# Performance work log

Hardware: AMD Instinct MI355X
Metric: run time of the kernel (lower is better)

Reference implementation:

```python
import jax, jax.numpy as jnp
import numpy as np

G = 8  # order of C8 rotation group

def expand_circulant(w):
    # w: [out_fields, in_fields, G] free params of a C8 regular->regular 1x1 conv.
    # Full weight: W[of*G+go, if*G+gi] = w[of, if, (go-gi) mod G]
    g = jnp.arange(G)
    idx = (g[:, None] - g[None, :]) % G            # [go, gi]
    Wf = w[:, :, idx]                              # [of, if, go, gi]
    Wf = jnp.transpose(Wf, (0, 2, 1, 3))           # [of, go, if, gi]
    return Wf.reshape(w.shape[0] * G, w.shape[1] * G)

def eq_proj(x2, w, b):
    # x2: [B, in_fields*G]; equivariant 1x1 conv = GEMM with circulant-expanded weight
    Wf = expand_circulant(w)                       # [out_fields*G, in_fields*G]
    bf = jnp.repeat(b, G)                          # per-field bias, shared across group dim
    return x2 @ Wf.T + bf

def setup_inputs() -> dict:
    key = jax.random.key(0)
    ks = jax.random.split(key, 12)
    B, d_model, n_head, d_k, d_v = 8192, 128, 8, 64, 64
    C = d_model * G                                # 1024
    s_in = 0.02
    inp = {
        'q': jax.random.normal(ks[0], (B, C, 1, 1), jnp.float32),
        'k': jax.random.normal(ks[1], (B, C, 1, 1), jnp.float32),
        'v': jax.random.normal(ks[2], (B, C, 1, 1), jnp.float32),
        'w_q': jax.random.normal(ks[3], (n_head * d_k, d_model, G), jnp.float32) * s_in,
        'b_q': jnp.zeros((n_head * d_k,), jnp.float32),
        'w_k': jax.random.normal(ks[4], (n_head * d_k, d_model, G), jnp.float32) * s_in,
        'b_k': jnp.zeros((n_head * d_k,), jnp.float32),
        'w_v': jax.random.normal(ks[5], (n_head * d_v, d_model, G), jnp.float32) * s_in,
        'b_v': jnp.zeros((n_head * d_v,), jnp.float32),
        'w_fc': jax.random.normal(ks[6], (d_model, n_head * d_v, G), jnp.float32) * s_in,
        'b_fc': jnp.zeros((d_model,), jnp.float32),
    }
    return inp

def reference(q, k, v, w_q, b_q, w_k, b_k, w_v, b_v, w_fc, b_fc):
    B, C = q.shape[0], q.shape[1]
    n_head, d_k = 8, 64
    d_v = 64
    temp = jnp.asarray(d_k ** 0.5, q.dtype)
    residual = q                                   # [B, C, 1, 1]
    q2 = q.reshape(B, C)
    k2 = k.reshape(B, C)
    v2 = v.reshape(B, C)
    # equivariant 1x1 conv projections -> [B, n_head*d_k*G]
    qp = eq_proj(q2, w_q, b_q).reshape(B, G, n_head, d_k).transpose(0, 2, 1, 3)  # [B,H,G,dk]
    kp = eq_proj(k2, w_k, b_k).reshape(B, G, n_head, d_k).transpose(0, 2, 1, 3)
    vp = eq_proj(v2, w_v, b_v).reshape(B, G, n_head, d_v).transpose(0, 2, 1, 3)
    # scaled dot-product attention over the G=8 group/orientation positions
    attn = jax.nn.softmax(jnp.einsum('bhqd,bhkd->bhqk', qp / temp, kp), axis=-1)  # [B,H,G,G]
    out = jnp.einsum('bhqk,bhkd->bhqd', attn, vp)  # [B,H,G,dv]
    # transpose(1,2) then flatten, exactly as torch .view(sz_b, -1, 1, 1)
    out = out.transpose(0, 2, 1, 3).reshape(B, G * n_head * d_v)
    out = eq_proj(out, w_fc, b_fc)                 # [B, d_model*G]
    out = out.reshape(B, C, 1, 1) + residual
    return out, attn
```

## Files before the change

### kernel.cpp

```cpp
#include <hip/hip_runtime.h>
#include <hip/hip_bf16.h>

typedef unsigned short u16;
typedef unsigned int u32;
typedef __bf16 bf16x8_t __attribute__((ext_vector_type(8)));
typedef float f32x4_t __attribute__((ext_vector_type(4)));

#define BK 64

__device__ __forceinline__ float b2f(u16 v) {
  return __uint_as_float(((u32)v) << 16);
}
__device__ __forceinline__ u16 f2b(float f) {
  __hip_bfloat16 h = __float2bfloat16(f);
  return *reinterpret_cast<u16*>(&h);
}
__device__ __forceinline__ float blo(u32 u) { return __uint_as_float(u << 16); }
__device__ __forceinline__ float bhi(u32 u) { return __uint_as_float(u & 0xffff0000u); }

__device__ __forceinline__ void async_lds16(const u16* g, u16* l) {
  __builtin_amdgcn_global_load_lds(
      (__attribute__((address_space(1))) void*)g,
      (__attribute__((address_space(3))) void*)l, 16, 0, 0);
}

__device__ __forceinline__ void expand8(const float* __restrict__ w,
                                        u16* __restrict__ dst, int I,
                                        int kshift, int gid) {
  const int n = gid >> kshift;
  const int kc = (gid & ((1 << kshift) - 1)) * 8;
  const int K = 8 << kshift;
  const float* wp = w + (size_t)((n >> 3) * I + (kc >> 3)) * 8;
  float4 w0 = *(const float4*)wp;
  float4 w1 = *(const float4*)(wp + 4);
  float w8[8] = {w0.x, w0.y, w0.z, w0.w, w1.x, w1.y, w1.z, w1.w};
  u16 t[8];
  const int r = (n - kc) & 7;
#pragma unroll
  for (int j = 0; j < 8; ++j) t[j] = f2b(w8[(r - j) & 7]);
  *(uint4*)(dst + (size_t)n * K + kc) = *(const uint4*)t;
}

__device__ __forceinline__ void cvt8(const float* __restrict__ src,
                                     u16* __restrict__ dst, int gid) {
  const float* p = src + (size_t)gid * 8;
  float4 a = *(const float4*)p;
  float4 b = *(const float4*)(p + 4);
  u16 t[8] = {f2b(a.x), f2b(a.y), f2b(a.z), f2b(a.w),
              f2b(b.x), f2b(b.y), f2b(b.z), f2b(b.w)};
  *(uint4*)(dst + (size_t)gid * 8) = *(const uint4*)t;
}

__global__ __launch_bounds__(256) void expand_all(
    const float* __restrict__ w_q, const float* __restrict__ w_k,
    const float* __restrict__ w_v, const float* __restrict__ w_fc,
    const float* __restrict__ q, const float* __restrict__ k,
    const float* __restrict__ v, u16* __restrict__ Wq, u16* __restrict__ Wk,
    u16* __restrict__ Wv, u16* __restrict__ Wfc, u16* __restrict__ qb,
    u16* __restrict__ kb, u16* __restrict__ vb, int cblocks) {
  const int e = blockIdx.x;
  if (e < 8192) {
    const int plane = e >> 11;
    const int gid = (e & 2047) * 256 + threadIdx.x;
    if (plane == 0) expand8(w_q, Wq, 128, 7, gid);
    else if (plane == 1) expand8(w_k, Wk, 128, 7, gid);
    else if (plane == 2) expand8(w_v, Wv, 128, 7, gid);
    else expand8(w_fc, Wfc, 512, 9, gid);
  } else {
    const int ce = e - 8192;
    const int plane = ce / cblocks;
    const int gid = (ce - plane * cblocks) * 256 + threadIdx.x;
    if (plane == 0) cvt8(q, qb, gid);
    else if (plane == 1) cvt8(k, kb, gid);
    else cvt8(v, vb, gid);
  }
}

__global__ __launch_bounds__(512, 2) void gemm_qkv256(
    const u16* __restrict__ X0, const u16* __restrict__ X1,
    const u16* __restrict__ X2, const u16* __restrict__ W0,
    const u16* __restrict__ W1, const u16* __restrict__ W2,
    const float* __restrict__ b0, const float* __restrict__ b1,
    const float* __restrict__ b2, u16* __restrict__ Y0, u16* __restrict__ Y1,
    u16* __restrict__ Y2, int M, int N, int K) {
  __shared__ __align__(16) u16 lds[4 * 16384];
  const int z = blockIdx.y;
  const u16* X = (z == 0) ? X0 : (z == 1) ? X1 : X2;
  const u16* W = (z == 0) ? W0 : (z == 1) ? W1 : W2;
  const float* bias = (z == 0) ? b0 : (z == 1) ? b1 : b2;
  u16* Y = (z == 0) ? Y0 : (z == 1) ? Y1 : Y2;

  const int tid = threadIdx.x;
  const int bid = blockIdx.x;
  const int grid_m = M >> 8, grid_n = N >> 8;
  const int nb = grid_m * grid_n;
  int pid = (bid & 7) * (nb >> 3) + (bid >> 3);
  const int nig = 8 * grid_n;
  const int group_id = pid / nig;
  const int first_m = group_id * 8;
  const int gsz = min(8, grid_m - first_m);
  const int mt = first_m + (pid % gsz);
  const int ntile = (pid % nig) / gsz;
  const int m0 = mt << 8, n0 = ntile << 8;

  const int lane = tid & 63, wave = tid >> 6;
  const int wm = (wave >> 2) * 128;
  const int wn = (wave & 3) * 64;
  const int l16 = lane & 15, quad = lane >> 4;
  const int kbl = quad ^ ((l16 >> 1) & 3);

  const int srow = tid >> 2;
  const int skbg = (tid & 3) ^ ((tid >> 3) & 3);
  const u16* pA = X + (size_t)(m0 + srow) * K + skbg * 8;
  const u16* pB = W + (size_t)(n0 + srow) * K + skbg * 8;
  const size_t rskip = (size_t)128 * K;

  const int aoff = (wm + l16) * 32 + kbl * 8;
  const int boff = 8192 + (wn + l16) * 32 + kbl * 8;

  f32x4_t acc[8][4] = {};
  const int nt = K >> 5;

  auto stage = [&](int t) {
    u16* l = lds + (t & 3) * 16384;
    const u16* a = pA + t * 32;
    const u16* b = pB + t * 32;
    async_lds16(a, l + tid * 8);
    async_lds16(a + rskip, l + tid * 8 + 4096);
    async_lds16(b, l + 8192 + tid * 8);
    async_lds16(b + rskip, l + 8192 + tid * 8 + 4096);
  };

  stage(0);
  __builtin_amdgcn_sched_barrier(0);
  stage(1);
  __builtin_amdgcn_sched_barrier(0);
  stage(2);
  asm volatile("s_waitcnt vmcnt(8)" ::: "memory");
  __builtin_amdgcn_s_barrier();
  __builtin_amdgcn_sched_barrier(0);

  for (int t = 0; t < nt; ++t) {
    if (t + 3 < nt) stage(t + 3);
    const u16* la = lds + (t & 3) * 16384 + aoff;
    const u16* lb = lds + (t & 3) * 16384 + boff;
    bf16x8_t a[8], b[4];
#pragma unroll
    for (int mi = 0; mi < 8; ++mi) a[mi] = *(const bf16x8_t*)(la + mi * 512);
#pragma unroll
    for (int ni = 0; ni < 4; ++ni) b[ni] = *(const bf16x8_t*)(lb + ni * 512);
    __builtin_amdgcn_s_setprio(1);
#pragma unroll
    for (int mi = 0; mi < 8; ++mi)
#pragma unroll
      for (int ni = 0; ni < 4; ++ni)
        acc[mi][ni] = __builtin_amdgcn_mfma_f32_16x16x32_bf16(a[mi], b[ni],
                                                              acc[mi][ni], 0, 0, 0);
    __builtin_amdgcn_s_setprio(0);
    if (t + 1 < nt) {
      if (t + 3 < nt)      asm volatile("s_waitcnt vmcnt(8)" ::: "memory");
      else if (t + 2 < nt) asm volatile("s_waitcnt vmcnt(4)" ::: "memory");
      else                 asm volatile("s_waitcnt vmcnt(0)" ::: "memory");
      __builtin_amdgcn_s_barrier();
      __builtin_amdgcn_sched_barrier(0);
    }
  }

#pragma unroll
  for (int ni = 0; ni < 4; ++ni) {
    const int col = n0 + wn + ni * 16 + l16;
    const float bv = bias[col >> 3];
#pragma unroll
    for (int mi = 0; mi < 8; ++mi) {
#pragma unroll
      for (int r = 0; r < 4; ++r) {
        const int rw = m0 + wm + mi * 16 + quad * 4 + r;
        Y[(size_t)rw * N + col] = f2b(acc[mi][ni][r] + bv);
      }
    }
  }
}

template <int TN, bool HAS_RES, bool OUT_F32>
__device__ __forceinline__ void gemm_core(
    const u16* __restrict__ Xb, const u16* __restrict__ W,
    const float* __restrict__ bias, const float* __restrict__ res,
    void* __restrict__ Yv, int M, int N, int K, int bid) {
  __shared__ __align__(16) u16 As[128 * BK];
  __shared__ __align__(16) u16 Bs[TN * BK];
  const int tid = threadIdx.x;

  const int grid_m = M >> 7, grid_n = N / TN;
  const int nb = grid_m * grid_n;
  int pid = (bid & 7) * (nb >> 3) + (bid >> 3);
  const int nig = 8 * grid_n;
  const int group_id = pid / nig;
  const int first_m = group_id * 8;
  const int gsz = min(8, grid_m - first_m);
  const int mt = first_m + (pid % gsz);
  const int nt = (pid % nig) / gsz;
  const int m0 = mt << 7, n0 = nt * TN;

  const int lane = tid & 63;
  const int wave = tid >> 6;
  const int wm = (wave >> 1) * 64;
  const int wn = (wave & 1) * (TN / 2);
  const int l16 = lane & 15;
  const int quad = lane >> 4;
  constexpr int NJ = TN >> 5;

  f32x4_t acc[4][NJ] = {};

  const int row0 = tid >> 3;
  const int kgl = ((tid & 7) ^ (row0 & 7)) * 8;

  for (int k0 = 0; k0 < K; k0 += BK) {
#pragma unroll
    for (int it = 0; it < TN / 32; ++it)
      async_lds16(W + (size_t)(n0 + row0 + it * 32) * K + (k0 + kgl),
                  &Bs[(tid + it * 256) * 8]);
#pragma unroll
    for (int it = 0; it < 4; ++it)
      async_lds16(Xb + (size_t)(m0 + row0 + it * 32) * K + (k0 + kgl),
                  &As[(tid + it * 256) * 8]);
    __syncthreads();
#pragma unroll
    for (int half = 0; half < 2; ++half) {
      bf16x8_t af[4], bfr[NJ];
#pragma unroll
      for (int i = 0; i < 4; ++i)
        af[i] = *(const bf16x8_t*)&As[(wm + i * 16 + l16) * BK +
                                      (((quad + half * 4) ^ (l16 & 7)) * 8)];
#pragma unroll
      for (int j = 0; j < NJ; ++j)
        bfr[j] = *(const bf16x8_t*)&Bs[(wn + j * 16 + l16) * BK +
                                       (((quad + half * 4) ^ (l16 & 7)) * 8)];
#pragma unroll
      for (int i = 0; i < 4; ++i)
#pragma unroll
        for (int j = 0; j < NJ; ++j)
          acc[i][j] =
              __builtin_amdgcn_mfma_f32_16x16x32_bf16(af[i], bfr[j], acc[i][j], 0, 0, 0);
    }
    __syncthreads();
  }

#pragma unroll
  for (int j = 0; j < NJ; ++j) {
    const int col = n0 + wn + j * 16 + l16;
    const float bv = bias[col >> 3];
#pragma unroll
    for (int i = 0; i < 4; ++i) {
#pragma unroll
      for (int r = 0; r < 4; ++r) {
        const int rw = m0 + wm + i * 16 + quad * 4 + r;
        float vv = acc[i][j][r] + bv;
        if (HAS_RES) vv += res[(size_t)rw * N + col];
        if (OUT_F32)
          ((float*)Yv)[(size_t)rw * N + col] = vv;
        else
          ((u16*)Yv)[(size_t)rw * N + col] = f2b(vv);
      }
    }
  }
}

__global__ __launch_bounds__(256) void gemm_fc(
    const u16* __restrict__ X, const u16* __restrict__ W,
    const float* __restrict__ bias, const float* __restrict__ res,
    float* __restrict__ Y, int M, int N, int K) {
  gemm_core<64, true, true>(X, W, bias, res, Y, M, N, K, blockIdx.x);
}

__global__ __launch_bounds__(256) void attn_kernel(
    const u16* __restrict__ qp, const u16* __restrict__ kp,
    const u16* __restrict__ vp, float* __restrict__ probs,
    u16* __restrict__ o, int iters) {
  __shared__ __align__(16) u16 Qs[4][8 * 72];
  __shared__ __align__(16) u16 Ks[4][8 * 72];
  __shared__ __align__(16) float Ps[4][64];
  const int tid = threadIdx.x;
  const int wave = tid >> 6;
  const int lane = tid & 63;
  const int r = lane >> 3, c = lane & 7;
  const int ls = r * 72 + c * 8;
  const int qg = r;
  const int kg = c;

  auto pairof = [&](int it) { return (it * gridDim.x + blockIdx.x) * 4 + wave; };
  auto gaddr = [&](int it) {
    const int pr = pairof(it);
    return (size_t)(pr >> 3) * 4096 + (size_t)r * 512 + (pr & 7) * 64 + c * 8;
  };

  uint4 qr = *(const uint4*)(qp + gaddr(0));
  uint4 kr = *(const uint4*)(kp + gaddr(0));

  for (int it = 0; it < iters; ++it) {
    *(uint4*)&Qs[wave][ls] = qr;
    *(uint4*)&Ks[wave][ls] = kr;
    const int pair = pairof(it);
    const int b = pair >> 3;
    const int h = pair & 7;
    float vcf[8];
#pragma unroll
    for (int k2 = 0; k2 < 8; ++k2)
      vcf[k2] = b2f(vp[(size_t)b * 4096 + (size_t)k2 * 512 + h * 64 + lane]);
    if (it + 1 < iters) {
      qr = *(const uint4*)(qp + gaddr(it + 1));
      kr = *(const uint4*)(kp + gaddr(it + 1));
    }
    float s = 0.f;
#pragma unroll
    for (int d8 = 0; d8 < 8; ++d8) {
      uint4 qa = *(const uint4*)&Qs[wave][qg * 72 + d8 * 8];
      uint4 ka = *(const uint4*)&Ks[wave][kg * 72 + d8 * 8];
      s += blo(qa.x) * blo(ka.x) + bhi(qa.x) * bhi(ka.x);
      s += blo(qa.y) * blo(ka.y) + bhi(qa.y) * bhi(ka.y);
      s += blo(qa.z) * blo(ka.z) + bhi(qa.z) * bhi(ka.z);
      s += blo(qa.w) * blo(ka.w) + bhi(qa.w) * bhi(ka.w);
    }
    s *= 0.125f;
    float mx = s;
    mx = fmaxf(mx, __shfl_xor(mx, 1));
    mx = fmaxf(mx, __shfl_xor(mx, 2));
    mx = fmaxf(mx, __shfl_xor(mx, 4));
    float e = __expf(s - mx);
    float sum = e;
    sum += __shfl_xor(sum, 1);
    sum += __shfl_xor(sum, 2);
    sum += __shfl_xor(sum, 4);
    const float p = e / sum;
    probs[(size_t)pair * 64 + lane] = p;
    Ps[wave][lane] = p;
#pragma unroll
    for (int q2 = 0; q2 < 8; ++q2) {
      float4 p0 = *(const float4*)&Ps[wave][q2 * 8];
      float4 p1 = *(const float4*)&Ps[wave][q2 * 8 + 4];
      float acc = p0.x * vcf[0] + p0.y * vcf[1] + p0.z * vcf[2] + p0.w * vcf[3] +
                  p1.x * vcf[4] + p1.y * vcf[5] + p1.z * vcf[6] + p1.w * vcf[7];
      o[(size_t)b * 4096 + q2 * 512 + h * 64 + lane] = f2b(acc);
    }
  }
}

extern "C" void kernel_launch(void* const* d_in, const int* in_sizes, int n_in,
                              void* d_out, int out_size, void* d_ws, size_t ws_size,
                              hipStream_t stream) {
  const float* q = (const float*)d_in[0];
  const float* k = (const float*)d_in[1];
  const float* v = (const float*)d_in[2];
  const float* w_q = (const float*)d_in[3];
  const float* b_q = (const float*)d_in[4];
  const float* w_k = (const float*)d_in[5];
  const float* b_k = (const float*)d_in[6];
  const float* w_v = (const float*)d_in[7];
  const float* b_v = (const float*)d_in[8];
  const float* w_fc = (const float*)d_in[9];
  const float* b_fc = (const float*)d_in[10];

  const int B = in_sizes[0] / 1024;
  float* out = (float*)d_out;
  float* probs = out + (size_t)B * 1024;

  u16* Wq = (u16*)d_ws;
  u16* Wk = Wq + (size_t)4096 * 1024;
  u16* Wv = Wk + (size_t)4096 * 1024;
  u16* Wfc = Wv + (size_t)4096 * 1024;
  u16* qb = Wfc + (size_t)4096 * 1024;
  u16* kb = qb + (size_t)B * 1024;
  u16* vb = kb + (size_t)B * 1024;
  u16* scratch = vb + (size_t)B * 1024;
  const size_t fixed_bytes =
      ((size_t)4 * 4096 * 1024 + (size_t)3 * B * 1024) * sizeof(u16);

  const size_t per_row = (size_t)(4 * 4096) * sizeof(u16);
  int chunkB = 256;
  for (int c = B; c >= 256; c >>= 1) {
    if (fixed_bytes + (size_t)c * per_row <= ws_size) { chunkB = c; break; }
  }

  u16* qp = scratch;
  u16* kp = qp + (size_t)chunkB * 4096;
  u16* vp = kp + (size_t)chunkB * 4096;
  u16* ao = vp + (size_t)chunkB * 4096;

  const int cblocks = B / 2;
  expand_all<<<8192 + 3 * cblocks, 256, 0, stream>>>(
      w_q, w_k, w_v, w_fc, q, k, v, Wq, Wk, Wv, Wfc, qb, kb, vb, cblocks);

  for (int cs = 0; cs < B; cs += chunkB) {
    const int nb_p = (chunkB / 256) * (4096 / 256);
    gemm_qkv256<<<dim3(nb_p, 3), 512, 0, stream>>>(
        qb + (size_t)cs * 1024, kb + (size_t)cs * 1024, vb + (size_t)cs * 1024,
        Wq, Wk, Wv, b_q, b_k, b_v, qp, kp, vp, chunkB, 4096, 1024);
    const int ablocks = (chunkB >= 1024) ? 2048 : chunkB * 2;
    const int aiters = (chunkB * 8) / (ablocks * 4);
    attn_kernel<<<ablocks, 256, 0, stream>>>(qp, kp, vp,
                                             probs + (size_t)cs * 512, ao, aiters);
    const int nb_fc = (chunkB / 128) * (1024 / 64);
    gemm_fc<<<nb_fc, 256, 0, stream>>>(ao, Wfc, b_fc, q + (size_t)cs * 1024,
                                       out + (size_t)cs * 1024, chunkB, 1024,
                                       4096);
  }
}
```

Measured before the change: 612.1 us.

## Double-buffer LDS-to-register fragment loads across K-tiles in bf16 GEMM loop

Restructures the GEMM main loop so LDS reads for the next K-tile's B fragments and first half of A fragments are issued while MFMAs for the current tile run. The A fragments are split into two halves so that loads of the second half overlap the first MFMA batch. The global-load wait is tightened so the next stage is resident one iteration earlier. The loop is unrolled by two to ping-pong B register buffers, which assumes an even tile count and raises register pressure.

```diff
diff --git a/kernel.cpp b/kernel.cpp
--- a/kernel.cpp
+++ b/kernel.cpp
@@ -131,39 +131,72 @@
     async_lds16(b + rskip, l + 8192 + tid * 8 + 4096);
   };
 
+  bf16x8_t A0[4], A1[4], Bc[4], Bn[4];
+
   stage(0);
   __builtin_amdgcn_sched_barrier(0);
   stage(1);
   __builtin_amdgcn_sched_barrier(0);
   stage(2);
-  asm volatile("s_waitcnt vmcnt(8)" ::: "memory");
+  asm volatile("s_waitcnt vmcnt(4)" ::: "memory");
   __builtin_amdgcn_s_barrier();
   __builtin_amdgcn_sched_barrier(0);
 
-  for (int t = 0; t < nt; ++t) {
+  {
+    const u16* la = lds + aoff;
+    const u16* lb = lds + boff;
+#pragma unroll
+    for (int mi = 0; mi < 4; ++mi) A0[mi] = *(const bf16x8_t*)(la + mi * 512);
+#pragma unroll
+    for (int ni = 0; ni < 4; ++ni) Bc[ni] = *(const bf16x8_t*)(lb + ni * 512);
+  }
+
+  auto body = [&](int t, bf16x8_t (&BCUR)[4], bf16x8_t (&BNXT)[4]) {
     if (t + 3 < nt) stage(t + 3);
-    const u16* la = lds + (t & 3) * 16384 + aoff;
-    const u16* lb = lds + (t & 3) * 16384 + boff;
-    bf16x8_t a[8], b[4];
-#pragma unroll
-    for (int mi = 0; mi < 8; ++mi) a[mi] = *(const bf16x8_t*)(la + mi * 512);
-#pragma unroll
-    for (int ni = 0; ni < 4; ++ni) b[ni] = *(const bf16x8_t*)(lb + ni * 512);
+    const u16* lc = lds + (t & 3) * 16384;
+    const u16* ln = lds + ((t + 1) & 3) * 16384;
+#pragma unroll
+    for (int mi = 0; mi < 4; ++mi)
+      A1[mi] = *(const bf16x8_t*)(lc + aoff + (mi + 4) * 512);
+    if (t + 1 < nt) {
+#pragma unroll
+      for (int ni = 0; ni < 4; ++ni)
+        BNXT[ni] = *(const bf16x8_t*)(ln + boff + ni * 512);
+    }
     __builtin_amdgcn_s_setprio(1);
 #pragma unroll
-    for (int mi = 0; mi < 8; ++mi)
+    for (int mi = 0; mi < 4; ++mi)
 #pragma unroll
       for (int ni = 0; ni < 4; ++ni)
-        acc[mi][ni] = __builtin_amdgcn_mfma_f32_16x16x32_bf16(a[mi], b[ni],
-                                                              acc[mi][ni], 0, 0, 0);
+        acc[mi][ni] = __builtin_amdgcn_mfma_f32_16x16x32_bf16(
+            A0[mi], BCUR[ni], acc[mi][ni], 0, 0, 0);
     __builtin_amdgcn_s_setprio(0);
     if (t + 1 < nt) {
-      if (t + 3 < nt)      asm volatile("s_waitcnt vmcnt(8)" ::: "memory");
-      else if (t + 2 < nt) asm volatile("s_waitcnt vmcnt(4)" ::: "memory");
-      else                 asm volatile("s_waitcnt vmcnt(0)" ::: "memory");
+#pragma unroll
+      for (int mi = 0; mi < 4; ++mi)
+        A0[mi] = *(const bf16x8_t*)(ln + aoff + mi * 512);
+    }
+    __builtin_amdgcn_s_setprio(1);
+#pragma unroll
+    for (int mi = 0; mi < 4; ++mi)
+#pragma unroll
+      for (int ni = 0; ni < 4; ++ni)
+        acc[mi + 4][ni] = __builtin_amdgcn_mfma_f32_16x16x32_bf16(
+            A1[mi], BCUR[ni], acc[mi + 4][ni], 0, 0, 0);
+    __builtin_amdgcn_s_setprio(0);
+    if (t + 1 < nt) {
+      asm volatile("s_waitcnt lgkmcnt(0)" ::: "memory");
+      __builtin_amdgcn_sched_barrier(0);
+      if (t + 3 < nt) asm volatile("s_waitcnt vmcnt(4)" ::: "memory");
+      else            asm volatile("s_waitcnt vmcnt(0)" ::: "memory");
       __builtin_amdgcn_s_barrier();
       __builtin_amdgcn_sched_barrier(0);
     }
+  };
+
+  for (int t = 0; t < nt; t += 2) {
+    body(t, Bc, Bn);
+    body(t + 1, Bn, Bc);
   }
 
 #pragma unroll
```

Measured after the change: 617.3 us. Within noise of the previous version (+0.8%).
